# Kernel tuning notes

Measured on AMD Instinct MI355X. Metric: run time of the kernel, lower is better.

## Reference

```python
import jax, jax.numpy as jnp
import numpy as np

B, N, C = 2, 30, 320
FH = FW = 64          # feature map (latent 128 / downsample 2)
PH = PW = 32          # roi_scale output size at this level
ORIG = 128.0          # original (latent) spatial size
SCALE = 0.5           # spatial_scale = 1/downsample_rate
SR = 2                # sampling_ratio
M = N + 1             # global channel + rois


def _bilinear(img, y, x):
    # img: (C, H, W); y, x: arbitrary-shape float coords. torchvision-style:
    # zero outside [-1, H]/[ -1, W], clamp then 4-corner interp.
    H, W = img.shape[1], img.shape[2]
    valid = (y > -1.0) & (y < H) & (x > -1.0) & (x < W)
    yc = jnp.clip(y, 0.0, H - 1.0)
    xc = jnp.clip(x, 0.0, W - 1.0)
    y0 = jnp.floor(yc).astype(jnp.int32)
    x0 = jnp.floor(xc).astype(jnp.int32)
    y1 = jnp.minimum(y0 + 1, H - 1)
    x1 = jnp.minimum(x0 + 1, W - 1)
    wy = yc - y0
    wx = xc - x0
    v = (img[:, y0, x0] * (1 - wy) * (1 - wx)
         + img[:, y0, x1] * (1 - wy) * wx
         + img[:, y1, x0] * wy * (1 - wx)
         + img[:, y1, x1] * wy * wx)
    return v * valid


def _roi_align_one(img, x1, y1, bw, bh):
    # img (C,FH,FW); x1,y1,bw,bh (N,) in aligned feature coords / bin sizes
    s = (jnp.arange(PH * SR, dtype=img.dtype) + 0.5) / SR   # sub-sample offsets in bin units
    yy = y1[:, None] + s[None, :] * bh[:, None]             # (N, PH*SR)
    xx = x1[:, None] + s[None, :] * bw[:, None]             # (N, PW*SR)
    yg = jnp.broadcast_to(yy[:, :, None], (N, PH * SR, PW * SR))
    xg = jnp.broadcast_to(xx[:, None, :], (N, PH * SR, PW * SR))
    v = _bilinear(img, yg, xg)                              # (C, N, PH*SR, PW*SR)
    v = v.reshape(C, N, PH, SR, PW, SR).mean(axis=(3, 5))   # average sub-samples
    return v.transpose(1, 0, 2, 3)                          # (N, C, PH, PW)


def _roi_unpool_one(roi_imgs, x1, y1, bw, bh):
    # inverse of roi_align: paste each (C,PH,PW) roi back into its own (FH,FW) map
    ys = jnp.arange(FH, dtype=roi_imgs.dtype)
    xs = jnp.arange(FW, dtype=roi_imgs.dtype)
    ry = (ys[None, :] - y1[:, None]) / bh[:, None] - 0.5    # (N, FH) roi-grid coords
    rx = (xs[None, :] - x1[:, None]) / bw[:, None] - 0.5    # (N, FW)
    ryg = jnp.broadcast_to(ry[:, :, None], (N, FH, FW))
    rxg = jnp.broadcast_to(rx[:, None, :], (N, FH, FW))
    return jax.vmap(_bilinear)(roi_imgs, ryg, rxg)          # (N, C, FH, FW); zeros outside box


def _fuser(x, perm, w_reduce, w1, b1, w2, b2):
    # FuseWeightGenerator: x (B, M, C, H, W)
    fg = jnp.sum(x, axis=2) != 0                            # (B, M, H, W) foreground mask
    fw = jnp.einsum('bmchw,c->bmhw', x, w_reduce)           # 1x1 conv C->1, no bias
    g = fw[:, :1]
    r = fw[:, 1:][:, perm]                                  # shuffle roi channels
    gin = jnp.concatenate([g, r], axis=1)                   # (B, M, H, W)
    # ChannelGate: only the 'max' branch affects the output (original uses last channel_att_raw)
    mp = gin.max(axis=(2, 3))                               # (B, M)
    att = jax.nn.relu(mp @ w1 + b1) @ w2 + b2
    gated = gin * jax.nn.sigmoid(att)[:, :, None, None]
    inv = jnp.argsort(perm)
    fw = jnp.concatenate([gated[:, :1], gated[:, 1:][:, inv]], axis=1)
    fw = jnp.where(fg, fw, jnp.finfo(fw.dtype).min)
    w = jax.nn.softmax(fw, axis=1)[:, :, None]              # (B, M, 1, H, W)
    return jnp.sum(x * w, axis=1)                           # (B, C, H, W)


def _forward(normed_hidden_states, attn_output, instance_boxes, instance_masks, perm,
             w_reduce, w1, b1, w2, b2):
    fmap = normed_hidden_states.reshape(B, FH, FW, C).transpose(0, 3, 1, 2)  # b c h w
    boxes = instance_boxes * ORIG * SCALE - 0.5             # aligned=True feature coords
    x1, y1 = boxes[..., 0], boxes[..., 1]
    x2, y2 = boxes[..., 2], boxes[..., 3]
    bw = (x2 - x1) / PW
    bh = (y2 - y1) / PH
    roi_feats = jax.vmap(_roi_align_one)(fmap, x1, y1, bw, bh)   # (B,N,C,PH,PW)
    mask = instance_masks.astype(roi_feats.dtype)[:, :, None, None, None]
    roi_feats = roi_feats * mask                             # masked rois stay zero
    unpooled = jax.vmap(_roi_unpool_one)(roi_feats, x1, y1, bw, bh) * mask  # (B,N,C,FH,FW)
    attn_map = attn_output.reshape(B, FH, FW, C).transpose(0, 3, 1, 2)[:, None]
    x = jnp.concatenate([attn_map, unpooled], axis=1)        # (B, M, C, FH, FW)
    fused = _fuser(x, perm, w_reduce, w1, b1, w2, b2)        # (B, C, FH, FW)
    return fused.transpose(0, 2, 3, 1).reshape(B, FH * FW, C)


def setup_inputs() -> dict:
    key = jax.random.key(0)
    ks = jax.random.split(key, 10)
    nhs = jax.random.normal(ks[0], (B, FH * FW, C), dtype=jnp.float32)
    attn = jax.random.normal(ks[1], (B, FH * FW, C), dtype=jnp.float32)
    cx = jax.random.uniform(ks[2], (B, N), minval=0.25, maxval=0.75)
    cy = jax.random.uniform(ks[3], (B, N), minval=0.25, maxval=0.75)
    hw = jax.random.uniform(ks[4], (B, N, 2), minval=0.1, maxval=0.4)
    boxes = jnp.stack([cx - hw[..., 0] / 2, cy - hw[..., 1] / 2,
                       cx + hw[..., 0] / 2, cy + hw[..., 1] / 2], axis=-1)
    boxes = jnp.clip(boxes, 0.0, 1.0).astype(jnp.float32)    # normalized xyxy
    masks = jax.random.randint(ks[5], (B, N), 0, 2).astype(jnp.int32)
    perm = jax.random.permutation(ks[6], N).astype(jnp.int32)
    w_reduce = (jax.random.normal(ks[7], (C,), dtype=jnp.float32) / np.sqrt(C)).astype(jnp.float32)
    w1 = (jax.random.normal(ks[8], (M, M), dtype=jnp.float32) / np.sqrt(M)).astype(jnp.float32)
    b1 = jnp.zeros((M,), dtype=jnp.float32)
    w2 = (jax.random.normal(ks[9], (M, M), dtype=jnp.float32) / np.sqrt(M)).astype(jnp.float32)
    b2 = jnp.zeros((M,), dtype=jnp.float32)
    return {"normed_hidden_states": nhs, "attn_output": attn, "instance_boxes": boxes,
            "instance_masks": masks, "perm": perm, "w_reduce": w_reduce,
            "w1": w1, "b1": b1, "w2": w2, "b2": b2}


def reference(normed_hidden_states, attn_output, instance_boxes, instance_masks, perm,
              w_reduce, w1, b1, w2, b2):
    return _forward(normed_hidden_states, attn_output, instance_boxes, instance_masks, perm,
                    w_reduce, w1, b1, w2, b2)
```

## Files before the change

### kernel.cpp

```cpp
#include <hip/hip_runtime.h>
#include <hip/hip_bf16.h>

#define NB 2
#define NN 30
#define NC 320
#define NM 31
#define HW 4096
#define FMIN_F (-3.40282346638528859812e+38f)
#define FCH 4

typedef float nfloat4 __attribute__((ext_vector_type(4)));

#define OFF_ASUM   0
#define OFF_AWRED  8192
#define OFF_RS     16384
#define OFF_RW     77824
#define OFF_MP     139264
#define WS_FLOATS  139328
#define ROIF_BYTE  557312

#define GRID_ROIF (NB * NN * 128)
#define GRID_RED  1639

__device__ __forceinline__ void get_box(const float* boxes, int b, int n,
                                        float& x1, float& y1, float& bw, float& bh) {
    const float* p = boxes + (b * NN + n) * 4;
    float X1 = p[0] * 64.0f - 0.5f;
    float Y1 = p[1] * 64.0f - 0.5f;
    float X2 = p[2] * 64.0f - 0.5f;
    float Y2 = p[3] * 64.0f - 0.5f;
    x1 = X1; y1 = Y1;
    bw = (X2 - X1) / 32.0f;
    bh = (Y2 - Y1) / 32.0f;
}

__device__ __forceinline__ unsigned short f2bf(float f) {
    __hip_bfloat16 h = __float2bfloat16(f);
    return *reinterpret_cast<unsigned short*>(&h);
}
__device__ __forceinline__ unsigned pack2(float a, float b) {
    return (unsigned)f2bf(a) | ((unsigned)f2bf(b) << 16);
}
__device__ __forceinline__ float blo(unsigned u) { return __uint_as_float(u << 16); }
__device__ __forceinline__ float bhi(unsigned u) { return __uint_as_float(u & 0xffff0000u); }

__device__ __forceinline__ unsigned encf(float f) {
    unsigned u = __float_as_uint(f);
    return (u & 0x80000000u) ? ~u : (u | 0x80000000u);
}
__device__ __forceinline__ float decf(unsigned e) {
    unsigned u = (e & 0x80000000u) ? (e & 0x7fffffffu) : ~e;
    return __uint_as_float(u);
}

__device__ void do_roifeat(int blk, const float* __restrict__ nhs,
                           const float* __restrict__ boxes,
                           const int* __restrict__ masks,
                           const float* __restrict__ wred,
                           float* __restrict__ ws,
                           unsigned* __restrict__ roif,
                           float* wsm , int* bsm ,
                           float* partS , float* partW ) {
    int bn = blk >> 7;
    int n = bn % NN;
    int b = bn / NN;
    if (masks[b * NN + n] == 0) return;
    int tid = threadIdx.x;
    float x1, y1, bw, bh;
    get_box(boxes, b, n, x1, y1, bw, bh);

    if (tid < 8) {
        int cell = blk * 8 + tid;
        int q = cell & 31;
        int p = (cell >> 5) & 31;
        float W[9] = {0.f,0.f,0.f,0.f,0.f,0.f,0.f,0.f,0.f};
        float wys[4], wxs[4];
        int iy0s[4], ix0s[4];
        int iymin = 64, ixmin = 64;
#pragma unroll
        for (int s_ = 0; s_ < 4; s_++) {
            int di = s_ >> 1, dj = s_ & 1;
            float y = y1 + ((float)p + 0.25f + 0.5f * (float)di) * bh;
            float x = x1 + ((float)q + 0.25f + 0.5f * (float)dj) * bw;
            float yc = fminf(fmaxf(y, 0.0f), 63.0f);
            float xc = fminf(fmaxf(x, 0.0f), 63.0f);
            int iy0 = (int)floorf(yc), ix0 = (int)floorf(xc);
            wys[s_] = yc - (float)iy0;
            wxs[s_] = xc - (float)ix0;
            iy0s[s_] = iy0; ix0s[s_] = ix0;
            iymin = min(iymin, iy0); ixmin = min(ixmin, ix0);
        }
#pragma unroll
        for (int s_ = 0; s_ < 4; s_++) {
            float wy = wys[s_], wx = wxs[s_];
            int dy = iy0s[s_] - iymin;
            int dx = ix0s[s_] - ixmin;
            bool yt = (iy0s[s_] == 63);
            bool xt = (ix0s[s_] == 63);
            float ay0 = yt ? 1.0f : (1.0f - wy);
            float ay1 = yt ? 0.0f : wy;
            float ax0 = xt ? 1.0f : (1.0f - wx);
            float ax1 = xt ? 0.0f : wx;
            float r0 = dy ? 0.0f : ay0;
            float r1 = dy ? ay0  : ay1;
            float r2 = dy ? ay1  : 0.0f;
            float c0 = dx ? 0.0f : ax0;
            float c1 = dx ? ax0  : ax1;
            float c2 = dx ? ax1  : 0.0f;
            W[0] += r0 * c0; W[1] += r0 * c1; W[2] += r0 * c2;
            W[3] += r1 * c0; W[4] += r1 * c1; W[5] += r1 * c2;
            W[6] += r2 * c0; W[7] += r2 * c1; W[8] += r2 * c2;
        }
#pragma unroll
        for (int k = 0; k < 9; k++) wsm[tid * 9 + k] = W[k] * 0.25f;
        bsm[tid] = iymin * 64 + ixmin;
    }
    __syncthreads();

    int cid = tid / 40;
    int v = tid - cid * 40;
    int cell = blk * 8 + cid;
    const float4* fb4 = (const float4*)(nhs + (size_t)b * HW * NC);
    int base = bsm[cid];
    float4 acc0 = make_float4(0.f, 0.f, 0.f, 0.f);
    float4 acc1 = make_float4(0.f, 0.f, 0.f, 0.f);
#pragma unroll
    for (int i = 0; i < 3; i++) {
#pragma unroll
        for (int j = 0; j < 3; j++) {
            float w = wsm[cid * 9 + i * 3 + j];
            if (w != 0.0f) {
                int off = (base + i * 64 + j) * 80 + v * 2;
                float4 f0 = fb4[off];
                float4 f1 = fb4[off + 1];
                acc0.x += w * f0.x; acc0.y += w * f0.y;
                acc0.z += w * f0.z; acc0.w += w * f0.w;
                acc1.x += w * f1.x; acc1.y += w * f1.y;
                acc1.z += w * f1.z; acc1.w += w * f1.w;
            }
        }
    }
    uint4 pk;
    pk.x = pack2(acc0.x, acc0.y);
    pk.y = pack2(acc0.z, acc0.w);
    pk.z = pack2(acc1.x, acc1.y);
    pk.w = pack2(acc1.z, acc1.w);
    ((uint4*)roif)[(size_t)cell * 40 + v] = pk;

    const float4* w4 = (const float4*)wred;
    float4 wv0 = w4[v * 2];
    float4 wv1 = w4[v * 2 + 1];
    partS[tid] = acc0.x + acc0.y + acc0.z + acc0.w + acc1.x + acc1.y + acc1.z + acc1.w;
    partW[tid] = acc0.x * wv0.x + acc0.y * wv0.y + acc0.z * wv0.z + acc0.w * wv0.w
               + acc1.x * wv1.x + acc1.y * wv1.y + acc1.z * wv1.z + acc1.w * wv1.w;
    __syncthreads();
    if (tid < 8) {
        float ss = 0.f, ww = 0.f;
#pragma unroll 8
        for (int k = 0; k < 40; k++) {
            ss += partS[tid * 40 + k];
            ww += partW[tid * 40 + k];
        }
        int c2 = blk * 8 + tid;
        ws[OFF_RS + c2] = ss;
        ws[OFF_RW + c2] = ww;
    }
}

__device__ void do_reduce(int rblk, const float* __restrict__ attn,
                          const float* __restrict__ wred, float* __restrict__ ws) {
    if (rblk == 0 && threadIdx.x < 64)
        ((unsigned*)(ws + OFF_MP))[threadIdx.x] = 0u;
    int wave = threadIdx.x >> 6;
    int lane = threadIdx.x & 63;
    int row = rblk * 5 + wave;
    if (row >= NB * HW) return;
    const float4* a4 = (const float4*)(attn + (size_t)row * NC);
    const float4* w4 = (const float4*)wred;
    float4 wv = w4[lane];
    float4 av = a4[lane];
    float s_a = av.x + av.y + av.z + av.w;
    float w_a = av.x * wv.x + av.y * wv.y + av.z * wv.z + av.w * wv.w;
    if (lane < 16) {
        float4 wv2 = w4[lane + 64];
        float4 av2 = a4[lane + 64];
        s_a += av2.x + av2.y + av2.z + av2.w;
        w_a += av2.x * wv2.x + av2.y * wv2.y + av2.z * wv2.z + av2.w * wv2.w;
    }
#pragma unroll
    for (int off = 32; off > 0; off >>= 1) {
        s_a += __shfl_down(s_a, off, 64);
        w_a += __shfl_down(w_a, off, 64);
    }
    if (lane == 0) {
        ws[OFF_ASUM + row]  = s_a;
        ws[OFF_AWRED + row] = w_a;
    }
}

__global__ void k_stage1(const float* __restrict__ nhs, const float* __restrict__ attn,
                         const float* __restrict__ boxes, const int* __restrict__ masks,
                         const float* __restrict__ wred, float* __restrict__ ws,
                         unsigned* __restrict__ roif) {
    __shared__ float wsm[72];
    __shared__ int bsm[8];
    __shared__ float partS[320], partW[320];
    int blk = blockIdx.x;
    if (blk < GRID_ROIF) {
        do_roifeat(blk, nhs, boxes, masks, wred, ws, roif, wsm, bsm, partS, partW);
    } else {
        do_reduce(blk - GRID_ROIF, attn, wred, ws);
    }
}

__global__ void k_fwmax(const float* __restrict__ boxes, const int* __restrict__ masks,
                        float* __restrict__ ws) {
    int unit = blockIdx.x;
    int bm = unit / FCH, ch = unit % FCH;
    int b = bm / NM, m = bm % NM;
    int pix0 = ch * (HW / FCH);
    int tid = threadIdx.x;
    float locmax = -INFINITY;
    if (m == 0) {
        for (int pix = pix0 + tid; pix < pix0 + HW / FCH; pix += 256)
            locmax = fmaxf(locmax, ws[OFF_AWRED + b * HW + pix]);
    } else {
        int n = m - 1;
        if (masks[b * NN + n]) {
            float x1, y1, bw, bh;
            get_box(boxes, b, n, x1, y1, bw, bh);
            const float* rw = ws + OFF_RW + (b * NN + n) * 1024;
            for (int pix = pix0 + tid; pix < pix0 + HW / FCH; pix += 256) {
                int h = pix >> 6, wp = pix & 63;
                float fwv = 0.0f;
                float ry = ((float)h - y1) / bh - 0.5f;
                float rx = ((float)wp - x1) / bw - 0.5f;
                bool valid = (ry > -1.0f) && (ry < 32.0f) && (rx > -1.0f) && (rx < 32.0f);
                if (valid) {
                    float yc = fminf(fmaxf(ry, 0.0f), 31.0f);
                    float xc = fminf(fmaxf(rx, 0.0f), 31.0f);
                    int iy0 = (int)floorf(yc), ix0 = (int)floorf(xc);
                    int iy1 = min(iy0 + 1, 31), ix1 = min(ix0 + 1, 31);
                    float wy = yc - (float)iy0, wx = xc - (float)ix0;
                    fwv = (1.f - wy) * (1.f - wx) * rw[iy0 * 32 + ix0]
                        + (1.f - wy) * wx * rw[iy0 * 32 + ix1]
                        + wy * (1.f - wx) * rw[iy1 * 32 + ix0]
                        + wy * wx * rw[iy1 * 32 + ix1];
                }
                locmax = fmaxf(locmax, fwv);
            }
        } else {
            locmax = 0.0f;
        }
    }
#pragma unroll
    for (int off = 32; off > 0; off >>= 1)
        locmax = fmaxf(locmax, __shfl_down(locmax, off, 64));
    __shared__ float red[4];
    int wid = tid >> 6, lane = tid & 63;
    if (lane == 0) red[wid] = locmax;
    __syncthreads();
    if (tid == 0) {
        float mx = fmaxf(fmaxf(red[0], red[1]), fmaxf(red[2], red[3]));
        atomicMax((unsigned*)(ws + OFF_MP) + bm, encf(mx));
    }
}

__global__ void k_final(const float* __restrict__ attn, const float* __restrict__ boxes,
                        const int* __restrict__ masks, const int* __restrict__ perm,
                        const float* __restrict__ w1, const float* __restrict__ b1,
                        const float* __restrict__ w2, const float* __restrict__ b2,
                        const float* __restrict__ ws, const unsigned* __restrict__ roif,
                        float* __restrict__ out) {
    __shared__ float mpg[NM], hb[NM], scal[32], wbuf[8][32];
    __shared__ int acnt[8];
    __shared__ unsigned char alist[8][NN];
    int t = threadIdx.x;
    int idx0 = blockIdx.x * 8;
    int b = idx0 >> 12;

    if (t < 8) acnt[t] = 0;
    if (t < NM) {
        unsigned e = ((const unsigned*)(ws + OFF_MP))[b * NM + ((t == 0) ? 0 : 1 + perm[t - 1])];
        mpg[t] = decf(e);
    }
    __syncthreads();
    if (t < NM) {
        float a = b1[t];
#pragma unroll
        for (int k = 0; k < NM; k++) a += mpg[k] * w1[k * NM + t];
        hb[t] = fmaxf(a, 0.0f);
    }
    __syncthreads();
    if (t < NM) {
        float a = b2[t];
#pragma unroll
        for (int k = 0; k < NM; k++) a += hb[k] * w2[k * NM + t];
        float sig = 1.0f / (1.0f + expf(-a));
        if (t == 0) scal[0] = sig;
        else        scal[1 + perm[t - 1]] = sig;
    }
    __syncthreads();

    if (t < 256) {
        int pg = t >> 5, m = t & 31;
        int pix = (idx0 + pg) & 4095;
        float zz = FMIN_F;
        if (m == 0) {
            float fwv = ws[OFF_AWRED + b * HW + pix];
            bool fg = (ws[OFF_ASUM + b * HW + pix] != 0.0f);
            zz = fg ? fwv * scal[0] : FMIN_F;
        } else if (m < NM) {
            int n = m - 1;
            if (masks[b * NN + n]) {
                float x1, y1, bw, bh;
                get_box(boxes, b, n, x1, y1, bw, bh);
                int h = pix >> 6, wp = pix & 63;
                float ry = ((float)h - y1) / bh - 0.5f;
                float rx = ((float)wp - x1) / bw - 0.5f;
                bool valid = (ry > -1.0f) && (ry < 32.0f) && (rx > -1.0f) && (rx < 32.0f);
                if (valid) {
                    float yc = fminf(fmaxf(ry, 0.0f), 31.0f);
                    float xc = fminf(fmaxf(rx, 0.0f), 31.0f);
                    int iy0 = (int)floorf(yc), ix0 = (int)floorf(xc);
                    int iy1 = min(iy0 + 1, 31), ix1 = min(ix0 + 1, 31);
                    float wy = yc - (float)iy0, wx = xc - (float)ix0;
                    float w00 = (1.f - wy) * (1.f - wx), w01 = (1.f - wy) * wx;
                    float w10 = wy * (1.f - wx), w11 = wy * wx;
                    const float* rw = ws + OFF_RW + (b * NN + n) * 1024;
                    const float* rs = ws + OFF_RS + (b * NN + n) * 1024;
                    float fwv = w00 * rw[iy0 * 32 + ix0] + w01 * rw[iy0 * 32 + ix1]
                              + w10 * rw[iy1 * 32 + ix0] + w11 * rw[iy1 * 32 + ix1];
                    float su  = w00 * rs[iy0 * 32 + ix0] + w01 * rs[iy0 * 32 + ix1]
                              + w10 * rs[iy1 * 32 + ix0] + w11 * rs[iy1 * 32 + ix1];
                    if (su != 0.0f) zz = fwv * scal[m];
                }
            }
        }
        float mx = zz;
#pragma unroll
        for (int off = 16; off > 0; off >>= 1)
            mx = fmaxf(mx, __shfl_xor(mx, off, 64));
        float e = (m < NM) ? expf(zz - mx) : 0.0f;
        float s = e;
#pragma unroll
        for (int off = 16; off > 0; off >>= 1)
            s += __shfl_xor(s, off, 64);
        if (m < NM) {
            float w = e / s;
            wbuf[pg][m] = w;
            if (m >= 1 && w != 0.0f) {
                int pos = atomicAdd(&acnt[pg], 1);
                alist[pg][pos] = (unsigned char)(m - 1);
            }
        }
    }
    __syncthreads();

    int pid = t / 40;
    int v = t - pid * 40;
    int idx = idx0 + pid;
    int pix = idx & 4095;
    int h = pix >> 6, wp = pix & 63;
    float w0 = wbuf[pid][0];
    const float4* at4 = (const float4*)attn;
    float4 a0 = at4[(size_t)idx * 80 + v * 2];
    float4 a1 = at4[(size_t)idx * 80 + v * 2 + 1];
    float4 acc0, acc1;
    acc0.x = a0.x * w0; acc0.y = a0.y * w0; acc0.z = a0.z * w0; acc0.w = a0.w * w0;
    acc1.x = a1.x * w0; acc1.y = a1.y * w0; acc1.z = a1.z * w0; acc1.w = a1.w * w0;
    const uint4* r4 = (const uint4*)roif;
    int na = acnt[pid];
    for (int k = 0; k < na; k++) {
        int n = alist[pid][k];
        float wn = wbuf[pid][n + 1];
        float x1, y1, bw, bh;
        get_box(boxes, b, n, x1, y1, bw, bh);
        float ry = ((float)h - y1) / bh - 0.5f;
        float rx = ((float)wp - x1) / bw - 0.5f;
        float yc = fminf(fmaxf(ry, 0.0f), 31.0f);
        float xc = fminf(fmaxf(rx, 0.0f), 31.0f);
        int iy0 = (int)floorf(yc), ix0 = (int)floorf(xc);
        int iy1 = min(iy0 + 1, 31), ix1 = min(ix0 + 1, 31);
        float wy = yc - (float)iy0, wx = xc - (float)ix0;
        float w00 = (1.f - wy) * (1.f - wx) * wn, w01 = (1.f - wy) * wx * wn;
        float w10 = wy * (1.f - wx) * wn, w11 = wy * wx * wn;
        size_t base = ((size_t)(b * NN + n)) << 10;
        uint4 U00 = r4[(base + iy0 * 32 + ix0) * 40 + v];
        uint4 U01 = r4[(base + iy0 * 32 + ix1) * 40 + v];
        uint4 U10 = r4[(base + iy1 * 32 + ix0) * 40 + v];
        uint4 U11 = r4[(base + iy1 * 32 + ix1) * 40 + v];
        acc0.x += w00 * blo(U00.x) + w01 * blo(U01.x) + w10 * blo(U10.x) + w11 * blo(U11.x);
        acc0.y += w00 * bhi(U00.x) + w01 * bhi(U01.x) + w10 * bhi(U10.x) + w11 * bhi(U11.x);
        acc0.z += w00 * blo(U00.y) + w01 * blo(U01.y) + w10 * blo(U10.y) + w11 * blo(U11.y);
        acc0.w += w00 * bhi(U00.y) + w01 * bhi(U01.y) + w10 * bhi(U10.y) + w11 * bhi(U11.y);
        acc1.x += w00 * blo(U00.z) + w01 * blo(U01.z) + w10 * blo(U10.z) + w11 * blo(U11.z);
        acc1.y += w00 * bhi(U00.z) + w01 * bhi(U01.z) + w10 * bhi(U10.z) + w11 * bhi(U11.z);
        acc1.z += w00 * blo(U00.w) + w01 * blo(U01.w) + w10 * blo(U10.w) + w11 * blo(U11.w);
        acc1.w += w00 * bhi(U00.w) + w01 * bhi(U01.w) + w10 * bhi(U10.w) + w11 * bhi(U11.w);
    }
    nfloat4 nv0 = { acc0.x, acc0.y, acc0.z, acc0.w };
    nfloat4 nv1 = { acc1.x, acc1.y, acc1.z, acc1.w };
    __builtin_nontemporal_store(nv0, ((nfloat4*)out) + (size_t)idx * 80 + v * 2);
    __builtin_nontemporal_store(nv1, ((nfloat4*)out) + (size_t)idx * 80 + v * 2 + 1);
}

extern "C" void kernel_launch(void* const* d_in, const int* in_sizes, int n_in,
                              void* d_out, int out_size, void* d_ws, size_t ws_size,
                              hipStream_t stream) {
    const float* nhs   = (const float*)d_in[0];
    const float* attn  = (const float*)d_in[1];
    const float* boxes = (const float*)d_in[2];
    const int*   masks = (const int*)d_in[3];
    const int*   perm  = (const int*)d_in[4];
    const float* wred  = (const float*)d_in[5];
    const float* w1    = (const float*)d_in[6];
    const float* b1    = (const float*)d_in[7];
    const float* w2    = (const float*)d_in[8];
    const float* b2    = (const float*)d_in[9];
    float* out = (float*)d_out;
    float* ws = (float*)d_ws;
    unsigned* roif = (unsigned*)((char*)d_ws + ROIF_BYTE);

    k_stage1<<<GRID_ROIF + GRID_RED, 320, 0, stream>>>(nhs, attn, boxes, masks, wred, ws, roif);
    k_fwmax<<<NB * NM * FCH, 256, 0, stream>>>(boxes, masks, ws);
    k_final<<<NB * HW / 8, 320, 0, stream>>>(attn, boxes, masks, perm, w1, b1, w2, b2, ws, roif, out);
}
```

Measured before the change: 118.2 us.

## Fuse per-ROI max into stage1 via last-block counter and drop k_fwmax

Removes the separate k_fwmax kernel. The global attention max is now folded into the reduce blocks with per-block atomicMax. The per-ROI unpooled max is computed by whichever of the 128 roifeat blocks for that ROI arrives last, detected with an atomic counter and threadfence, using the ROI weights staged in shared memory and only the pixels inside the box's bounding range. A memset now clears the max and counter slots each call. This saves a kernel launch and a full-map scan, at the cost of extra shared memory per block and a serialized tail for the last block of each ROI.

```diff
diff --git a/kernel.cpp b/kernel.cpp
--- a/kernel.cpp
+++ b/kernel.cpp
@@ -7,7 +7,6 @@
 #define NM 31
 #define HW 4096
 #define FMIN_F (-3.40282346638528859812e+38f)
-#define FCH 4
 
 typedef float nfloat4 __attribute__((ext_vector_type(4)));
 
@@ -16,8 +15,9 @@
 #define OFF_RS     16384
 #define OFF_RW     77824
 #define OFF_MP     139264
-#define WS_FLOATS  139328
-#define ROIF_BYTE  557312
+#define OFF_CNT    139328
+#define WS_FLOATS  139392
+#define ROIF_BYTE  557568
 
 #define GRID_ROIF (NB * NN * 128)
 #define GRID_RED  1639
@@ -60,7 +60,8 @@
                            float* __restrict__ ws,
                            unsigned* __restrict__ roif,
                            float* wsm , int* bsm ,
-                           float* partS , float* partW ) {
+                           float* partS , float* partW ,
+                           float* rwsm , int* lastf) {
     int bn = blk >> 7;
     int n = bn % NN;
     int b = bn / NN;
@@ -165,36 +166,107 @@
         ws[OFF_RS + c2] = ss;
         ws[OFF_RW + c2] = ww;
     }
+    __syncthreads();
+
+    if (tid == 0) {
+        __threadfence();
+        unsigned old = atomicAdd((unsigned*)(ws + OFF_CNT) + (b * NN + n), 1u);
+        int lf = (old == 127u);
+        if (lf) __threadfence();
+        *lastf = lf;
+    }
+    __syncthreads();
+    if (!*lastf) return;
+
+    const float* rw = ws + OFF_RW + (b * NN + n) * 1024;
+    for (int i = tid; i < 1024; i += 320) rwsm[i] = rw[i];
+    __syncthreads();
+
+    int h0  = max(0, (int)floorf(y1 - 0.5f * bh) - 1);
+    int h1  = min(63, (int)ceilf(y1 + 32.5f * bh) + 1);
+    int wq0 = max(0, (int)floorf(x1 - 0.5f * bw) - 1);
+    int wq1 = min(63, (int)ceilf(x1 + 32.5f * bw) + 1);
+    int Wd = wq1 - wq0 + 1;
+    int tot = Wd * (h1 - h0 + 1);
+    float lm = FMIN_F;
+    for (int i = tid; i < tot; i += 320) {
+        int h  = h0 + i / Wd;
+        int wp = wq0 + i % Wd;
+        float ry = ((float)h - y1) / bh - 0.5f;
+        float rx = ((float)wp - x1) / bw - 0.5f;
+        if (ry > -1.0f && ry < 32.0f && rx > -1.0f && rx < 32.0f) {
+            float yc = fminf(fmaxf(ry, 0.0f), 31.0f);
+            float xc = fminf(fmaxf(rx, 0.0f), 31.0f);
+            int iy0 = (int)floorf(yc), ix0 = (int)floorf(xc);
+            int iy1 = min(iy0 + 1, 31), ix1 = min(ix0 + 1, 31);
+            float wy = yc - (float)iy0, wx = xc - (float)ix0;
+            float fwv = (1.f - wy) * (1.f - wx) * rwsm[iy0 * 32 + ix0]
+                      + (1.f - wy) * wx        * rwsm[iy0 * 32 + ix1]
+                      + wy * (1.f - wx)        * rwsm[iy1 * 32 + ix0]
+                      + wy * wx                * rwsm[iy1 * 32 + ix1];
+            lm = fmaxf(lm, fwv);
+        }
+    }
+#pragma unroll
+    for (int off = 32; off > 0; off >>= 1)
+        lm = fmaxf(lm, __shfl_down(lm, off, 64));
+    int wid = tid >> 6;
+    if ((tid & 63) == 0) partS[wid] = lm;
+    __syncthreads();
+    if (tid == 0) {
+        float mx = fmaxf(fmaxf(fmaxf(partS[0], partS[1]),
+                               fmaxf(partS[2], partS[3])), partS[4]);
+        atomicMax((unsigned*)(ws + OFF_MP) + b * NM + 1 + n, encf(mx));
+    }
 }
 
 __device__ void do_reduce(int rblk, const float* __restrict__ attn,
-                          const float* __restrict__ wred, float* __restrict__ ws) {
-    if (rblk == 0 && threadIdx.x < 64)
-        ((unsigned*)(ws + OFF_MP))[threadIdx.x] = 0u;
+                          const float* __restrict__ wred, float* __restrict__ ws,
+                          float* redm , int* redb ) {
     int wave = threadIdx.x >> 6;
     int lane = threadIdx.x & 63;
     int row = rblk * 5 + wave;
-    if (row >= NB * HW) return;
-    const float4* a4 = (const float4*)(attn + (size_t)row * NC);
-    const float4* w4 = (const float4*)wred;
-    float4 wv = w4[lane];
-    float4 av = a4[lane];
-    float s_a = av.x + av.y + av.z + av.w;
-    float w_a = av.x * wv.x + av.y * wv.y + av.z * wv.z + av.w * wv.w;
-    if (lane < 16) {
-        float4 wv2 = w4[lane + 64];
-        float4 av2 = a4[lane + 64];
-        s_a += av2.x + av2.y + av2.z + av2.w;
-        w_a += av2.x * wv2.x + av2.y * wv2.y + av2.z * wv2.z + av2.w * wv2.w;
-    }
-#pragma unroll
-    for (int off = 32; off > 0; off >>= 1) {
-        s_a += __shfl_down(s_a, off, 64);
-        w_a += __shfl_down(w_a, off, 64);
+    bool act = (row < NB * HW);
+    float w_red = FMIN_F;
+    if (act) {
+        const float4* a4 = (const float4*)(attn + (size_t)row * NC);
+        const float4* w4 = (const float4*)wred;
+        float4 wv = w4[lane];
+        float4 av = a4[lane];
+        float s_a = av.x + av.y + av.z + av.w;
+        float w_a = av.x * wv.x + av.y * wv.y + av.z * wv.z + av.w * wv.w;
+        if (lane < 16) {
+            float4 wv2 = w4[lane + 64];
+            float4 av2 = a4[lane + 64];
+            s_a += av2.x + av2.y + av2.z + av2.w;
+            w_a += av2.x * wv2.x + av2.y * wv2.y + av2.z * wv2.z + av2.w * wv2.w;
+        }
+#pragma unroll
+        for (int off = 32; off > 0; off >>= 1) {
+            s_a += __shfl_down(s_a, off, 64);
+            w_a += __shfl_down(w_a, off, 64);
+        }
+        if (lane == 0) {
+            ws[OFF_ASUM + row]  = s_a;
+            ws[OFF_AWRED + row] = w_a;
+            w_red = w_a;
+        }
     }
     if (lane == 0) {
-        ws[OFF_ASUM + row]  = s_a;
-        ws[OFF_AWRED + row] = w_a;
+        redm[wave] = w_red;
+        redb[wave] = act ? (row >> 12) : -1;
+    }
+    __syncthreads();
+    if (threadIdx.x == 0) {
+        float m0 = FMIN_F, m1 = FMIN_F;
+#pragma unroll
+        for (int k = 0; k < 5; k++) {
+            if (redb[k] == 0)      m0 = fmaxf(m0, redm[k]);
+            else if (redb[k] == 1) m1 = fmaxf(m1, redm[k]);
+        }
+        unsigned* MP = (unsigned*)(ws + OFF_MP);
+        if (m0 > FMIN_F) atomicMax(MP + 0,  encf(m0));
+        if (m1 > FMIN_F) atomicMax(MP + NM, encf(m1));
     }
 }
 
@@ -205,64 +277,14 @@
     __shared__ float wsm[72];
     __shared__ int bsm[8];
     __shared__ float partS[320], partW[320];
+    __shared__ float rwsm[1024];
+    __shared__ int lastf;
     int blk = blockIdx.x;
     if (blk < GRID_ROIF) {
-        do_roifeat(blk, nhs, boxes, masks, wred, ws, roif, wsm, bsm, partS, partW);
+        do_roifeat(blk, nhs, boxes, masks, wred, ws, roif,
+                   wsm, bsm, partS, partW, rwsm, &lastf);
     } else {
-        do_reduce(blk - GRID_ROIF, attn, wred, ws);
-    }
-}
-
-__global__ void k_fwmax(const float* __restrict__ boxes, const int* __restrict__ masks,
-                        float* __restrict__ ws) {
-    int unit = blockIdx.x;
-    int bm = unit / FCH, ch = unit % FCH;
-    int b = bm / NM, m = bm % NM;
-    int pix0 = ch * (HW / FCH);
-    int tid = threadIdx.x;
-    float locmax = -INFINITY;
-    if (m == 0) {
-        for (int pix = pix0 + tid; pix < pix0 + HW / FCH; pix += 256)
-            locmax = fmaxf(locmax, ws[OFF_AWRED + b * HW + pix]);
-    } else {
-        int n = m - 1;
-        if (masks[b * NN + n]) {
-            float x1, y1, bw, bh;
-            get_box(boxes, b, n, x1, y1, bw, bh);
-            const float* rw = ws + OFF_RW + (b * NN + n) * 1024;
-            for (int pix = pix0 + tid; pix < pix0 + HW / FCH; pix += 256) {
-                int h = pix >> 6, wp = pix & 63;
-                float fwv = 0.0f;
-                float ry = ((float)h - y1) / bh - 0.5f;
-                float rx = ((float)wp - x1) / bw - 0.5f;
-                bool valid = (ry > -1.0f) && (ry < 32.0f) && (rx > -1.0f) && (rx < 32.0f);
-                if (valid) {
-                    float yc = fminf(fmaxf(ry, 0.0f), 31.0f);
-                    float xc = fminf(fmaxf(rx, 0.0f), 31.0f);
-                    int iy0 = (int)floorf(yc), ix0 = (int)floorf(xc);
-                    int iy1 = min(iy0 + 1, 31), ix1 = min(ix0 + 1, 31);
-                    float wy = yc - (float)iy0, wx = xc - (float)ix0;
-                    fwv = (1.f - wy) * (1.f - wx) * rw[iy0 * 32 + ix0]
-                        + (1.f - wy) * wx * rw[iy0 * 32 + ix1]
-                        + wy * (1.f - wx) * rw[iy1 * 32 + ix0]
-                        + wy * wx * rw[iy1 * 32 + ix1];
-                }
-                locmax = fmaxf(locmax, fwv);
-            }
-        } else {
-            locmax = 0.0f;
-        }
-    }
-#pragma unroll
-    for (int off = 32; off > 0; off >>= 1)
-        locmax = fmaxf(locmax, __shfl_down(locmax, off, 64));
-    __shared__ float red[4];
-    int wid = tid >> 6, lane = tid & 63;
-    if (lane == 0) red[wid] = locmax;
-    __syncthreads();
-    if (tid == 0) {
-        float mx = fmaxf(fmaxf(red[0], red[1]), fmaxf(red[2], red[3]));
-        atomicMax((unsigned*)(ws + OFF_MP) + bm, encf(mx));
+        do_reduce(blk - GRID_ROIF, attn, wred, ws, partS, bsm);
     }
 }
 
@@ -282,7 +304,8 @@
     if (t < 8) acnt[t] = 0;
     if (t < NM) {
         unsigned e = ((const unsigned*)(ws + OFF_MP))[b * NM + ((t == 0) ? 0 : 1 + perm[t - 1])];
-        mpg[t] = decf(e);
+        float v = (e == 0u) ? 0.0f : decf(e);
+        mpg[t] = (t == 0) ? v : fmaxf(v, 0.0f);
     }
     __syncthreads();
     if (t < NM) {
@@ -422,7 +445,7 @@
     float* ws = (float*)d_ws;
     unsigned* roif = (unsigned*)((char*)d_ws + ROIF_BYTE);
 
+    hipMemsetAsync((char*)d_ws + OFF_MP * 4, 0, 512, stream);
     k_stage1<<<GRID_ROIF + GRID_RED, 320, 0, stream>>>(nhs, attn, boxes, masks, wred, ws, roif);
-    k_fwmax<<<NB * NM * FCH, 256, 0, stream>>>(boxes, masks, ws);
     k_final<<<NB * HW / 8, 320, 0, stream>>>(attn, boxes, masks, perm, w1, b1, w2, b2, ws, roif, out);
 }
```

Result: slower. 246.2 us (+108.3%).
